# Optimization experiments

Hardware: AMD Instinct MI355X
Metric: run time of the kernel (lower is better)

## Reference

```python
import jax, jax.numpy as jnp
import numpy as np

EPS = 1e-6
B, T, E, H = 2, 512, 1024, 256
NUM_BLOCK = 12


def normalize(x):
    # RMS-style normalization over the feature dim (no learned affine)
    return x * jax.lax.rsqrt(jnp.mean(x * x, axis=-1, keepdims=True) + EPS)


def bar_quadratic_causal(a, b):
    # y_i = (1/i) * sum_{j<=i} relu(a_i + b_j)   (causal prefix mean of pairwise relation)
    # a, b: [B, T, H]
    Tn = a.shape[1]
    pair = jax.nn.relu(a[:, :, None, :] + b[:, None, :, :])  # [B, T(i), T(j), H]
    mask = jnp.tril(jnp.ones((Tn, Tn), dtype=a.dtype))        # causal j<=i
    s = jnp.einsum('bijh,ij->bih', pair, mask)
    counts = jnp.arange(1, Tn + 1, dtype=a.dtype)[None, :, None]
    return s / counts


def setup_inputs() -> dict:
    key = jax.random.key(0)
    k0, k1, k2, k3 = jax.random.split(key, 4)
    x = jax.random.normal(k0, (B, T, E), dtype=jnp.float32)
    w1 = jax.random.normal(k1, (E, H), dtype=jnp.float32) * 0.02
    b1 = jnp.zeros((H,), dtype=jnp.float32)
    w2 = jax.random.normal(k2, (E, H), dtype=jnp.float32) * 0.02
    b2 = jnp.zeros((H,), dtype=jnp.float32)
    w3 = jax.random.normal(k3, (H, E), dtype=jnp.float32) * (0.02 / np.sqrt(NUM_BLOCK))
    b3 = jnp.zeros((E,), dtype=jnp.float32)
    return {"x": x, "w1": w1, "b1": b1, "w2": w2, "b2": b2, "w3": w3, "b3": b3}


def reference(x, w1, b1, w2, b2, w3, b3):
    r = normalize(x)
    a = r @ w1 + b1
    b = r @ w2 + b2
    # PreNorm == 'approx': normalize a and b separately
    a = normalize(a)
    b = normalize(b)
    r = bar_quadratic_causal(a, b)
    # PostNorm == 'yes'
    r = normalize(r)
    r = r @ w3 + b3
    return x + r
```

## Files before the change

kernel.cpp:

```cpp
#include <hip/hip_runtime.h>

#define EPSF 1e-6f
#define Bsz 2
#define Tn  512
#define En  1024
#define Hn  256
#define Mtot (Bsz * Tn)
typedef unsigned short us_t;
typedef unsigned int   u32_t;

typedef __attribute__((ext_vector_type(8))) short bf16x8;
typedef __attribute__((ext_vector_type(4))) float f32x4;
#define MFMA16(a, b, c) __builtin_amdgcn_mfma_f32_16x16x32_bf16((a), (b), (c), 0, 0, 0)

__device__ __forceinline__ us_t f2bf(float f) {
  union { float f; u32_t u; } x; x.f = f;
  u32_t r = (x.u + 0x7fffu + ((x.u >> 16) & 1u)) >> 16;
  return (us_t)r;
}
__device__ __forceinline__ float bf2f(us_t u) {
  union { u32_t u; float f; } x; x.u = ((u32_t)u) << 16; return x.f;
}
__device__ __forceinline__ uint2 pack4bf(float a, float b, float c, float d) {
  uint2 r;
  r.x = (u32_t)f2bf(a) | ((u32_t)f2bf(b) << 16);
  r.y = (u32_t)f2bf(c) | ((u32_t)f2bf(d) << 16);
  return r;
}
__device__ __forceinline__ float block_reduce_sum_256(float v, float* smem) {
  #pragma unroll
  for (int off = 32; off > 0; off >>= 1) v += __shfl_down(v, off, 64);
  const int wave = threadIdx.x >> 6;
  if ((threadIdx.x & 63) == 0) smem[wave] = v;
  __syncthreads();
  float s = smem[0] + smem[1] + smem[2] + smem[3];
  __syncthreads();
  return s;
}

__global__ __launch_bounds__(256) void k_castx_rs(
    const float* __restrict__ x, us_t* __restrict__ xb, float* __restrict__ rs)
{
  __shared__ float red[4];
  const int row = blockIdx.x, t = threadIdx.x;
  float4 v = ((const float4*)(x + (size_t)row * En))[t];
  float ss = block_reduce_sum_256(v.x*v.x + v.y*v.y + v.z*v.z + v.w*v.w, red);
  if (t == 0) rs[row] = rsqrtf(ss * (1.0f / En) + EPSF);
  ((uint2*)(xb + (size_t)row * En))[t] = pack4bf(v.x, v.y, v.z, v.w);
}

__global__ __launch_bounds__(256) void k_tr(
    const float* __restrict__ w1, const float* __restrict__ w2,
    const float* __restrict__ w3,
    us_t* __restrict__ w1t, us_t* __restrict__ w2t, us_t* __restrict__ w3t)
{
  const int b = blockIdx.x, t = threadIdx.x;
  const float* src; us_t* dst; int R, C, tr, tc;
  if (b < 256)      { src = w1; dst = w1t; R = 1024; C = 256;  tr = b >> 3;  tc = b & 7; }
  else if (b < 512) { int i = b - 256; src = w2; dst = w2t; R = 1024; C = 256; tr = i >> 3; tc = i & 7; }
  else              { int i = b - 512; src = w3; dst = w3t; R = 256; C = 1024; tr = i >> 5; tc = i & 31; }

  __shared__ float ts[32][33];
  const int r = t >> 3, c4 = (t & 7) * 4;
  float4 v = *(const float4*)(src + (size_t)(tr * 32 + r) * C + tc * 32 + c4);
  ts[r][c4 + 0] = v.x; ts[r][c4 + 1] = v.y; ts[r][c4 + 2] = v.z; ts[r][c4 + 3] = v.w;
  __syncthreads();
  float o0 = ts[c4 + 0][r], o1 = ts[c4 + 1][r], o2 = ts[c4 + 2][r], o3 = ts[c4 + 3][r];
  *(uint2*)(dst + (size_t)(tc * 32 + r) * R + tr * 32 + c4) = pack4bf(o0, o1, o2, o3);
}

__global__ __launch_bounds__(256) void k_gemm_ab(
    const us_t* __restrict__ xb,
    const us_t* __restrict__ w1t, const us_t* __restrict__ w2t,
    float* __restrict__ P)
{
  const int wid = threadIdx.x >> 6, lane = threadIdx.x & 63;
  const int wg = blockIdx.x * 4 + wid;
  const int ks = wg & 3, nt = (wg >> 2) & 15, mt = wg >> 6;
  const int m0 = mt * 32, n0 = nt * 32, k0 = ks * 256;
  const int lg = lane >> 4, lr = lane & 15;

  const us_t* ap0 = xb + (size_t)(m0 + lr) * En + k0 + lg * 8;
  const us_t* ap1 = ap0 + 16 * En;
  const us_t* bbase = (n0 < Hn) ? (w1t + (size_t)n0 * En) : (w2t + (size_t)(n0 - Hn) * En);
  const us_t* bp0 = bbase + (size_t)lr * En + k0 + lg * 8;
  const us_t* bp1 = bp0 + 16 * En;

  f32x4 acc00 = {0.f,0.f,0.f,0.f}, acc01 = acc00, acc10 = acc00, acc11 = acc00;

  #pragma unroll 4
  for (int s = 0; s < 8; ++s) {
    bf16x8 a0 = *(const bf16x8*)(ap0 + s * 32);
    bf16x8 a1 = *(const bf16x8*)(ap1 + s * 32);
    bf16x8 b0 = *(const bf16x8*)(bp0 + s * 32);
    bf16x8 b1 = *(const bf16x8*)(bp1 + s * 32);
    acc00 = MFMA16(a0, b0, acc00);
    acc01 = MFMA16(a0, b1, acc01);
    acc10 = MFMA16(a1, b0, acc10);
    acc11 = MFMA16(a1, b1, acc11);
  }

  float* pw = P + ((size_t)ks * Mtot + m0 + lg * 4) * 512 + n0 + lr;
  #pragma unroll
  for (int i = 0; i < 4; ++i) {
    pw[(size_t)i        * 512      ] = acc00[i];
    pw[(size_t)i        * 512 + 16 ] = acc01[i];
    pw[(size_t)(i + 16) * 512      ] = acc10[i];
    pw[(size_t)(i + 16) * 512 + 16 ] = acc11[i];
  }
}

__global__ __launch_bounds__(256) void k_norm(
    const float* __restrict__ P, const float* __restrict__ rs,
    const float* __restrict__ b1, const float* __restrict__ b2,
    us_t* __restrict__ A, us_t* __restrict__ Bm)
{
  const int rw = blockIdx.x * 4 + (threadIdx.x >> 6);
  const int lane = threadIdx.x & 63;
  const int which = rw >> 10, r = rw & 1023;
  const float* bias = which ? b2 : b1;
  const int h0 = lane * 4;
  const size_t off = (size_t)r * 512 + which * Hn + h0;
  const size_t KS = (size_t)Mtot * 512;

  float4 d0 = *(const float4*)(P + off);
  float4 d1 = *(const float4*)(P + off + KS);
  float4 d2 = *(const float4*)(P + off + 2 * KS);
  float4 d3 = *(const float4*)(P + off + 3 * KS);
  const float sc0 = rs[r];
  float4 bv = *(const float4*)(bias + h0);
  float vx = (d0.x + d1.x + d2.x + d3.x) * sc0 + bv.x;
  float vy = (d0.y + d1.y + d2.y + d3.y) * sc0 + bv.y;
  float vz = (d0.z + d1.z + d2.z + d3.z) * sc0 + bv.z;
  float vw = (d0.w + d1.w + d2.w + d3.w) * sc0 + bv.w;

  float ss = vx*vx + vy*vy + vz*vz + vw*vw;
  #pragma unroll
  for (int off2 = 32; off2 > 0; off2 >>= 1) ss += __shfl_xor(ss, off2, 64);
  const float sc = rsqrtf(ss * (1.0f / Hn) + EPSF);

  us_t* outp = which ? Bm : A;
  *(uint2*)(outp + (size_t)r * Hn + h0) = pack4bf(vx * sc, vy * sc, vz * sc, vw * sc);
}

#define ITILE 2
#define JCH   16
__global__ __launch_bounds__(256) void k_bar(
    const us_t* __restrict__ A, const us_t* __restrict__ Bm,
    us_t* __restrict__ Yb)
{
  const int tile = blockIdx.x & 255;
  const int bb   = blockIdx.x >> 8;
  const int i0   = tile * ITILE;
  const int h    = threadIdx.x;
  const size_t base = (size_t)bb * Tn * Hn;
  const us_t* __restrict__ bp = Bm + base + h;

  float av[ITILE], sum[ITILE];
  #pragma unroll
  for (int r = 0; r < ITILE; ++r) {
    av[r]  = bf2f(A[base + (size_t)(i0 + r) * Hn + h]);
    sum[r] = 0.f;
  }

  const int nfull = i0 & ~(JCH - 1);
  us_t b0[JCH], b1[JCH];

  #define LOADCH(buf, jj) { _Pragma("unroll") \
    for (int tt = 0; tt < JCH; ++tt) buf[tt] = bp[(size_t)((jj) + tt) * Hn]; }
  #define COMPCH(buf) { _Pragma("unroll") \
    for (int tt = 0; tt < JCH; ++tt) { float bv = bf2f(buf[tt]); _Pragma("unroll") \
      for (int r = 0; r < ITILE; ++r) sum[r] += fmaxf(av[r] + bv, 0.f); } }

  if (nfull > 0) {
    LOADCH(b0, 0);
    int j = 0;
    while (true) {
      const bool more1 = (j + JCH     < nfull);
      const bool more2 = (j + 2 * JCH < nfull);
      if (more1) LOADCH(b1, j + JCH);
      COMPCH(b0);
      j += JCH;
      if (!more1) break;
      if (more2) LOADCH(b0, j + JCH);
      COMPCH(b1);
      j += JCH;
      if (!more2) break;
    }
  }
  {
    us_t bt[JCH];
    LOADCH(bt, nfull);
    const int lim = i0 - nfull;
    #pragma unroll
    for (int tt = 0; tt < JCH; ++tt) {
      float bv = bf2f(bt[tt]);
      #pragma unroll
      for (int r = 0; r < ITILE; ++r)
        sum[r] += (tt <= lim + r) ? fmaxf(av[r] + bv, 0.f) : 0.f;
    }
  }
  #undef LOADCH
  #undef COMPCH

  __shared__ float red[4];
  #pragma unroll
  for (int r = 0; r < ITILE; ++r) {
    float ss = block_reduce_sum_256(sum[r] * sum[r], red);
    float c  = (float)(i0 + r + 1);
    float sc = rsqrtf(ss * (1.0f / Hn) + EPSF * c * c);
    Yb[base + (size_t)(i0 + r) * Hn + h] = f2bf(sum[r] * sc);
  }
}

__global__ __launch_bounds__(256) void k_out(
    const us_t* __restrict__ Yb, const us_t* __restrict__ w3t,
    const float* __restrict__ x, const float* __restrict__ b3,
    float* __restrict__ out)
{
  const int wid = threadIdx.x >> 6, lane = threadIdx.x & 63;
  const int wg = blockIdx.x * 4 + wid;
  const int nt = wg & 31, mt = wg >> 5;
  const int m0 = mt * 16, n0 = nt * 32;
  const int lg = lane >> 4, lr = lane & 15;

  const us_t* ap  = Yb  + (size_t)(m0 + lr) * Hn + lg * 8;
  const us_t* bp0 = w3t + (size_t)(n0 + lr) * Hn + lg * 8;
  const us_t* bp1 = bp0 + 16 * Hn;

  f32x4 acc0 = {0.f,0.f,0.f,0.f}, acc1 = acc0;

  #pragma unroll 4
  for (int s = 0; s < 8; ++s) {
    bf16x8 a  = *(const bf16x8*)(ap  + s * 32);
    bf16x8 b0 = *(const bf16x8*)(bp0 + s * 32);
    bf16x8 b1 = *(const bf16x8*)(bp1 + s * 32);
    acc0 = MFMA16(a, b0, acc0);
    acc1 = MFMA16(a, b1, acc1);
  }

  const int row = m0 + lg * 4;
  const int c0 = n0 + lr, c1 = n0 + 16 + lr;
  const float bv0 = b3[c0], bv1 = b3[c1];
  #pragma unroll
  for (int i = 0; i < 4; ++i) {
    const size_t o0 = (size_t)(row + i) * En + c0;
    const size_t o1 = (size_t)(row + i) * En + c1;
    out[o0] = x[o0] + acc0[i] + bv0;
    out[o1] = x[o1] + acc1[i] + bv1;
  }
}

extern "C" void kernel_launch(void* const* d_in, const int* in_sizes, int n_in,
                              void* d_out, int out_size, void* d_ws, size_t ws_size,
                              hipStream_t stream) {
  const float* x  = (const float*)d_in[0];
  const float* w1 = (const float*)d_in[1];
  const float* b1 = (const float*)d_in[2];
  const float* w2 = (const float*)d_in[3];
  const float* b2 = (const float*)d_in[4];
  const float* w3 = (const float*)d_in[5];
  const float* b3 = (const float*)d_in[6];
  float* out = (float*)d_out;

  char* p = (char*)d_ws;
  float* P   = (float*)p;               p += (size_t)4 * Mtot * 512 * 4;
  us_t* xb   = (us_t*)p;                p += (size_t)Mtot * En * 2;
  us_t* w1t  = (us_t*)p;                p += (size_t)Hn * En * 2;
  us_t* w2t  = (us_t*)p;                p += (size_t)Hn * En * 2;
  us_t* w3t  = (us_t*)p;                p += (size_t)En * Hn * 2;
  us_t* A    = (us_t*)p;                p += (size_t)Mtot * Hn * 2;
  us_t* Bm   = (us_t*)p;                p += (size_t)Mtot * Hn * 2;
  us_t* Yb   = (us_t*)p;                p += (size_t)Mtot * Hn * 2;
  float* rs  = (float*)p;               p += (size_t)Mtot * 4;

  k_castx_rs<<<Mtot, 256, 0, stream>>>(x, xb, rs);
  k_tr      <<<768,  256, 0, stream>>>(w1, w2, w3, w1t, w2t, w3t);
  k_gemm_ab <<<512,  256, 0, stream>>>(xb, w1t, w2t, P);
  k_norm    <<<512,  256, 0, stream>>>(P, rs, b1, b2, A, Bm);
  k_bar     <<<Bsz * (Tn / ITILE), 256, 0, stream>>>(A, Bm, Yb);
  k_out     <<<512,  256, 0, stream>>>(Yb, w3t, x, b3, out);
}
```

Before: 53.30 us.

## Fuse prep kernels, fold norm into GEMM epilogue, reverse bar tile order

Merges the x cast/rms kernel and the weight-transpose kernel into one launch. Drops the split-K GEMM and its 8 MB fp32 partial buffer: each block now computes full-K for 32 rows by 256 columns and does the bias plus RMS normalization in an LDS epilogue. Reverses the tile order for the second batch in k_bar so long and short causal rows are mixed across the grid, and doubles the M tile in the output GEMM. The trade-off is that the fused GEMM runs only 64 blocks with a 32-step K loop, which may underuse the GPU.

```diff
diff --git a/kernel.cpp b/kernel.cpp
--- a/kernel.cpp
+++ b/kernel.cpp
@@ -38,29 +38,31 @@
   return s;
 }
 
-__global__ __launch_bounds__(256) void k_castx_rs(
-    const float* __restrict__ x, us_t* __restrict__ xb, float* __restrict__ rs)
-{
-  __shared__ float red[4];
-  const int row = blockIdx.x, t = threadIdx.x;
-  float4 v = ((const float4*)(x + (size_t)row * En))[t];
-  float ss = block_reduce_sum_256(v.x*v.x + v.y*v.y + v.z*v.z + v.w*v.w, red);
-  if (t == 0) rs[row] = rsqrtf(ss * (1.0f / En) + EPSF);
-  ((uint2*)(xb + (size_t)row * En))[t] = pack4bf(v.x, v.y, v.z, v.w);
-}
-
-__global__ __launch_bounds__(256) void k_tr(
+__global__ __launch_bounds__(256) void k_prep(
+    const float* __restrict__ x,
     const float* __restrict__ w1, const float* __restrict__ w2,
     const float* __restrict__ w3,
+    us_t* __restrict__ xb, float* __restrict__ rs,
     us_t* __restrict__ w1t, us_t* __restrict__ w2t, us_t* __restrict__ w3t)
 {
+  __shared__ float red[4];
+  __shared__ float ts[32][33];
   const int b = blockIdx.x, t = threadIdx.x;
+
+  if (b < 1024) {
+    float4 v = ((const float4*)(x + (size_t)b * En))[t];
+    float ss = block_reduce_sum_256(v.x*v.x + v.y*v.y + v.z*v.z + v.w*v.w, red);
+    if (t == 0) rs[b] = rsqrtf(ss * (1.0f / En) + EPSF);
+    ((uint2*)(xb + (size_t)b * En))[t] = pack4bf(v.x, v.y, v.z, v.w);
+    return;
+  }
+
+  const int i = b - 1024;
   const float* src; us_t* dst; int R, C, tr, tc;
-  if (b < 256)      { src = w1; dst = w1t; R = 1024; C = 256;  tr = b >> 3;  tc = b & 7; }
-  else if (b < 512) { int i = b - 256; src = w2; dst = w2t; R = 1024; C = 256; tr = i >> 3; tc = i & 7; }
-  else              { int i = b - 512; src = w3; dst = w3t; R = 256; C = 1024; tr = i >> 5; tc = i & 31; }
-
-  __shared__ float ts[32][33];
+  if (i < 256)      { src = w1; dst = w1t; R = 1024; C = 256;  tr = i >> 3;  tc = i & 7; }
+  else if (i < 512) { int k = i - 256; src = w2; dst = w2t; R = 1024; C = 256; tr = k >> 3; tc = k & 7; }
+  else              { int k = i - 512; src = w3; dst = w3t; R = 256; C = 1024; tr = k >> 5; tc = k & 31; }
+
   const int r = t >> 3, c4 = (t & 7) * 4;
   float4 v = *(const float4*)(src + (size_t)(tr * 32 + r) * C + tc * 32 + c4);
   ts[r][c4 + 0] = v.x; ts[r][c4 + 1] = v.y; ts[r][c4 + 2] = v.z; ts[r][c4 + 3] = v.w;
@@ -69,78 +71,66 @@
   *(uint2*)(dst + (size_t)(tc * 32 + r) * R + tr * 32 + c4) = pack4bf(o0, o1, o2, o3);
 }
 
-__global__ __launch_bounds__(256) void k_gemm_ab(
+__global__ __launch_bounds__(512) void k_gemm_ab(
     const us_t* __restrict__ xb,
     const us_t* __restrict__ w1t, const us_t* __restrict__ w2t,
-    float* __restrict__ P)
-{
-  const int wid = threadIdx.x >> 6, lane = threadIdx.x & 63;
-  const int wg = blockIdx.x * 4 + wid;
-  const int ks = wg & 3, nt = (wg >> 2) & 15, mt = wg >> 6;
-  const int m0 = mt * 32, n0 = nt * 32, k0 = ks * 256;
-  const int lg = lane >> 4, lr = lane & 15;
-
-  const us_t* ap0 = xb + (size_t)(m0 + lr) * En + k0 + lg * 8;
-  const us_t* ap1 = ap0 + 16 * En;
-  const us_t* bbase = (n0 < Hn) ? (w1t + (size_t)n0 * En) : (w2t + (size_t)(n0 - Hn) * En);
-  const us_t* bp0 = bbase + (size_t)lr * En + k0 + lg * 8;
-  const us_t* bp1 = bp0 + 16 * En;
-
-  f32x4 acc00 = {0.f,0.f,0.f,0.f}, acc01 = acc00, acc10 = acc00, acc11 = acc00;
-
-  #pragma unroll 4
-  for (int s = 0; s < 8; ++s) {
-    bf16x8 a0 = *(const bf16x8*)(ap0 + s * 32);
-    bf16x8 a1 = *(const bf16x8*)(ap1 + s * 32);
-    bf16x8 b0 = *(const bf16x8*)(bp0 + s * 32);
-    bf16x8 b1 = *(const bf16x8*)(bp1 + s * 32);
-    acc00 = MFMA16(a0, b0, acc00);
-    acc01 = MFMA16(a0, b1, acc01);
-    acc10 = MFMA16(a1, b0, acc10);
-    acc11 = MFMA16(a1, b1, acc11);
-  }
-
-  float* pw = P + ((size_t)ks * Mtot + m0 + lg * 4) * 512 + n0 + lr;
-  #pragma unroll
-  for (int i = 0; i < 4; ++i) {
-    pw[(size_t)i        * 512      ] = acc00[i];
-    pw[(size_t)i        * 512 + 16 ] = acc01[i];
-    pw[(size_t)(i + 16) * 512      ] = acc10[i];
-    pw[(size_t)(i + 16) * 512 + 16 ] = acc11[i];
-  }
-}
-
-__global__ __launch_bounds__(256) void k_norm(
-    const float* __restrict__ P, const float* __restrict__ rs,
+    const float* __restrict__ rs,
     const float* __restrict__ b1, const float* __restrict__ b2,
     us_t* __restrict__ A, us_t* __restrict__ Bm)
 {
-  const int rw = blockIdx.x * 4 + (threadIdx.x >> 6);
-  const int lane = threadIdx.x & 63;
-  const int which = rw >> 10, r = rw & 1023;
-  const float* bias = which ? b2 : b1;
-  const int h0 = lane * 4;
-  const size_t off = (size_t)r * 512 + which * Hn + h0;
-  const size_t KS = (size_t)Mtot * 512;
-
-  float4 d0 = *(const float4*)(P + off);
-  float4 d1 = *(const float4*)(P + off + KS);
-  float4 d2 = *(const float4*)(P + off + 2 * KS);
-  float4 d3 = *(const float4*)(P + off + 3 * KS);
-  const float sc0 = rs[r];
-  float4 bv = *(const float4*)(bias + h0);
-  float vx = (d0.x + d1.x + d2.x + d3.x) * sc0 + bv.x;
-  float vy = (d0.y + d1.y + d2.y + d3.y) * sc0 + bv.y;
-  float vz = (d0.z + d1.z + d2.z + d3.z) * sc0 + bv.z;
-  float vw = (d0.w + d1.w + d2.w + d3.w) * sc0 + bv.w;
-
-  float ss = vx*vx + vy*vy + vz*vz + vw*vw;
-  #pragma unroll
-  for (int off2 = 32; off2 > 0; off2 >>= 1) ss += __shfl_xor(ss, off2, 64);
+  const int blk   = blockIdx.x;
+  const int which = blk & 1;
+  const int m0    = (blk >> 1) * 32;
+  const int w     = threadIdx.x >> 6;
+  const int lane  = threadIdx.x & 63;
+  const int rh    = w >> 2;
+  const int nq    = w & 3;
+  const int n0    = nq * 64;
+  const int lg    = lane >> 4, lr = lane & 15;
+
+  const us_t* __restrict__ wt = which ? w2t : w1t;
+  const us_t* ap = xb + (size_t)(m0 + rh * 16 + lr) * En + lg * 8;
+  const us_t* bp = wt + (size_t)(n0 + lr) * En + lg * 8;
+
+  f32x4 acc[4];
+  #pragma unroll
+  for (int c = 0; c < 4; ++c) acc[c] = (f32x4){0.f, 0.f, 0.f, 0.f};
+
+  #pragma unroll 4
+  for (int s = 0; s < 32; ++s) {
+    bf16x8 a = *(const bf16x8*)(ap + s * 32);
+    #pragma unroll
+    for (int c = 0; c < 4; ++c) {
+      bf16x8 bb = *(const bf16x8*)(bp + (size_t)c * 16 * En + s * 32);
+      acc[c] = MFMA16(a, bb, acc[c]);
+    }
+  }
+
+  __shared__ float sv[32][260];
+  #pragma unroll
+  for (int c = 0; c < 4; ++c)
+    #pragma unroll
+    for (int i = 0; i < 4; ++i)
+      sv[rh * 16 + lg * 4 + i][n0 + c * 16 + lr] = acc[c][i];
+  __syncthreads();
+
+  const int row = threadIdx.x >> 4, seg = threadIdx.x & 15;
+  const float rscale = rs[m0 + row];
+  const float* __restrict__ bias = which ? b2 : b1;
+  float v[16]; float ss = 0.f;
+  #pragma unroll
+  for (int k = 0; k < 16; ++k) {
+    float val = sv[row][seg * 16 + k] * rscale + bias[seg * 16 + k];
+    v[k] = val; ss += val * val;
+  }
+  #pragma unroll
+  for (int off = 1; off < 16; off <<= 1) ss += __shfl_xor(ss, off, 64);
   const float sc = rsqrtf(ss * (1.0f / Hn) + EPSF);
 
-  us_t* outp = which ? Bm : A;
-  *(uint2*)(outp + (size_t)r * Hn + h0) = pack4bf(vx * sc, vy * sc, vz * sc, vw * sc);
+  us_t* outp = (which ? Bm : A) + (size_t)(m0 + row) * Hn + seg * 16;
+  #pragma unroll
+  for (int k = 0; k < 4; ++k)
+    ((uint2*)outp)[k] = pack4bf(v[4*k] * sc, v[4*k+1] * sc, v[4*k+2] * sc, v[4*k+3] * sc);
 }
 
 #define ITILE 2
@@ -149,9 +139,10 @@
     const us_t* __restrict__ A, const us_t* __restrict__ Bm,
     us_t* __restrict__ Yb)
 {
-  const int tile = blockIdx.x & 255;
-  const int bb   = blockIdx.x >> 8;
-  const int i0   = tile * ITILE;
+  const int raw  = blockIdx.x;
+  const int sel  = (raw < 256) ? raw : (511 - raw);
+  const int bb   = raw >> 8;
+  const int i0   = sel * ITILE;
   const int h    = threadIdx.x;
   const size_t base = (size_t)bb * Tn * Hn;
   const us_t* __restrict__ bp = Bm + base + h;
@@ -221,33 +212,39 @@
   const int wid = threadIdx.x >> 6, lane = threadIdx.x & 63;
   const int wg = blockIdx.x * 4 + wid;
   const int nt = wg & 31, mt = wg >> 5;
-  const int m0 = mt * 16, n0 = nt * 32;
+  const int m0 = mt * 32, n0 = nt * 32;
   const int lg = lane >> 4, lr = lane & 15;
 
-  const us_t* ap  = Yb  + (size_t)(m0 + lr) * Hn + lg * 8;
+  const us_t* ap0 = Yb  + (size_t)(m0 + lr) * Hn + lg * 8;
+  const us_t* ap1 = ap0 + 16 * Hn;
   const us_t* bp0 = w3t + (size_t)(n0 + lr) * Hn + lg * 8;
   const us_t* bp1 = bp0 + 16 * Hn;
 
-  f32x4 acc0 = {0.f,0.f,0.f,0.f}, acc1 = acc0;
+  f32x4 acc00 = {0.f,0.f,0.f,0.f}, acc01 = acc00, acc10 = acc00, acc11 = acc00;
 
   #pragma unroll 4
   for (int s = 0; s < 8; ++s) {
-    bf16x8 a  = *(const bf16x8*)(ap  + s * 32);
+    bf16x8 a0 = *(const bf16x8*)(ap0 + s * 32);
+    bf16x8 a1 = *(const bf16x8*)(ap1 + s * 32);
     bf16x8 b0 = *(const bf16x8*)(bp0 + s * 32);
     bf16x8 b1 = *(const bf16x8*)(bp1 + s * 32);
-    acc0 = MFMA16(a, b0, acc0);
-    acc1 = MFMA16(a, b1, acc1);
-  }
-
-  const int row = m0 + lg * 4;
+    acc00 = MFMA16(a0, b0, acc00);
+    acc01 = MFMA16(a0, b1, acc01);
+    acc10 = MFMA16(a1, b0, acc10);
+    acc11 = MFMA16(a1, b1, acc11);
+  }
+
   const int c0 = n0 + lr, c1 = n0 + 16 + lr;
   const float bv0 = b3[c0], bv1 = b3[c1];
   #pragma unroll
   for (int i = 0; i < 4; ++i) {
-    const size_t o0 = (size_t)(row + i) * En + c0;
-    const size_t o1 = (size_t)(row + i) * En + c1;
-    out[o0] = x[o0] + acc0[i] + bv0;
-    out[o1] = x[o1] + acc1[i] + bv1;
+    const int r0 = m0 + lg * 4 + i, r1 = r0 + 16;
+    const size_t o00 = (size_t)r0 * En + c0, o01 = (size_t)r0 * En + c1;
+    const size_t o10 = (size_t)r1 * En + c0, o11 = (size_t)r1 * En + c1;
+    out[o00] = x[o00] + acc00[i] + bv0;
+    out[o01] = x[o01] + acc01[i] + bv1;
+    out[o10] = x[o10] + acc10[i] + bv0;
+    out[o11] = x[o11] + acc11[i] + bv1;
   }
 }
 
@@ -264,7 +261,6 @@
   float* out = (float*)d_out;
 
   char* p = (char*)d_ws;
-  float* P   = (float*)p;               p += (size_t)4 * Mtot * 512 * 4;
   us_t* xb   = (us_t*)p;                p += (size_t)Mtot * En * 2;
   us_t* w1t  = (us_t*)p;                p += (size_t)Hn * En * 2;
   us_t* w2t  = (us_t*)p;                p += (size_t)Hn * En * 2;
@@ -274,10 +270,8 @@
   us_t* Yb   = (us_t*)p;                p += (size_t)Mtot * Hn * 2;
   float* rs  = (float*)p;               p += (size_t)Mtot * 4;
 
-  k_castx_rs<<<Mtot, 256, 0, stream>>>(x, xb, rs);
-  k_tr      <<<768,  256, 0, stream>>>(w1, w2, w3, w1t, w2t, w3t);
-  k_gemm_ab <<<512,  256, 0, stream>>>(xb, w1t, w2t, P);
-  k_norm    <<<512,  256, 0, stream>>>(P, rs, b1, b2, A, Bm);
-  k_bar     <<<Bsz * (Tn / ITILE), 256, 0, stream>>>(A, Bm, Yb);
-  k_out     <<<512,  256, 0, stream>>>(Yb, w3t, x, b3, out);
-}
+  k_prep    <<<1792, 256, 0, stream>>>(x, w1, w2, w3, xb, rs, w1t, w2t, w3t);
+  k_gemm_ab <<<64,   512, 0, stream>>>(xb, w1t, w2t, rs, b1, b2, A, Bm);
+  k_bar     <<<512,  256, 0, stream>>>(A, Bm, Yb);
+  k_out     <<<256,  256, 0, stream>>>(Yb, w3t, x, b3, out);
+}
```

Result: slower. 77.63 us (+45.7%).
